# Kernel optimization log

Measured on AMD Instinct MI355X. Metric: run time of the kernel, lower is better.

## Reference

```python
import jax, jax.numpy as jnp
import numpy as np

IMAGE_SIZE = 256
VIEW_ANGLE = 30.0 * np.pi / 180.0  # NMR default viewing angle
SIGMA = 1e-2                        # softness of the differentiable coverage test
EPS = 1e-6


def setup_inputs() -> dict:
    key = jax.random.key(0)
    k1, k2, k3 = jax.random.split(key, 3)
    V, F = 502, 1000
    # normalize_vertices -> points on/near the unit sphere centered at origin
    verts = jax.random.normal(k1, (1, V, 3), dtype=jnp.float32)
    verts = verts / (jnp.linalg.norm(verts, axis=-1, keepdims=True) + EPS)
    faces = jax.random.randint(k2, (1, F, 3), 0, V, dtype=jnp.int32)
    camera_position = jnp.array([6.0, 10.0, -14.0], dtype=jnp.float32)
    # binary silhouette reference, as produced by (image.max(-1) > 0.1)
    image_ref = (jax.random.uniform(k3, (1, IMAGE_SIZE, IMAGE_SIZE)) > 0.5).astype(jnp.float32)
    return {"vertices": verts, "faces": faces, "camera_position": camera_position, "image_ref": image_ref}


def _look_at(vertices, eye):
    # camera_mode='look_at': at=origin, up=+y
    at = jnp.zeros(3, dtype=vertices.dtype)
    up = jnp.array([0.0, 1.0, 0.0], dtype=vertices.dtype)
    z = at - eye
    z = z / (jnp.linalg.norm(z) + EPS)
    x = jnp.cross(up, z)
    x = x / (jnp.linalg.norm(x) + EPS)
    y = jnp.cross(z, x)
    R = jnp.stack([x, y, z], axis=0)           # [3,3], rows are camera axes
    return jnp.einsum('bvj,ij->bvi', vertices - eye, R)  # [1,V,3]


def _render_silhouette(vertices, faces, eye):
    H = W = IMAGE_SIZE
    v = _look_at(vertices, eye)                # [1,V,3] camera space
    w = jnp.tan(jnp.asarray(VIEW_ANGLE, v.dtype))
    zc = v[..., 2]
    proj = jnp.stack([v[..., 0] / (zc * w), v[..., 1] / (zc * w)], axis=-1)  # [1,V,2] NDC xy
    fv = proj[0][faces[0]]                     # [F,3,2] projected triangle vertices
    v0, v1, v2 = fv[:, 0], fv[:, 1], fv[:, 2]

    # pixel centers in NDC, row 0 at top (y=+)
    xs = (2.0 * jnp.arange(W, dtype=v.dtype) + 1.0) / W - 1.0
    ys = 1.0 - (2.0 * jnp.arange(H, dtype=v.dtype) + 1.0) / H
    px = jnp.stack(jnp.meshgrid(xs, ys, indexing='xy'), axis=-1).reshape(-1, 2)  # [P,2]

    def edge_sdist(a, b):
        # signed distance of every pixel to line a->b, computed as px @ n^T - (a.n)
        e = b - a                                           # [F,2]
        n = jnp.stack([-e[:, 1], e[:, 0]], axis=-1)
        n = n / (jnp.linalg.norm(e, axis=-1, keepdims=True) + EPS)
        return px @ n.T - jnp.sum(a * n, axis=-1)[None, :]  # [P,F]

    # orient consistently via signed triangle area
    e01, e02 = v1 - v0, v2 - v0
    area = e01[:, 0] * e02[:, 1] - e01[:, 1] * e02[:, 0]    # [F]
    s = jnp.sign(area)[None, :]

    inv_sigma = 1.0 / SIGMA
    frag = (jax.nn.sigmoid(edge_sdist(v0, v1) * s * inv_sigma)
            * jax.nn.sigmoid(edge_sdist(v1, v2) * s * inv_sigma)
            * jax.nn.sigmoid(edge_sdist(v2, v0) * s * inv_sigma))  # [P,F] soft coverage

    sil = 1.0 - jnp.prod(1.0 - frag, axis=1)                # soft-or over faces, [P]
    return sil.reshape(1, H, W)


def reference(vertices, faces, camera_position, image_ref):
    image = _render_silhouette(vertices, faces, camera_position)  # [1,H,W]
    loss = jnp.sum((image - image_ref) ** 2)
    return loss
```

## Files before the change

### kernel.cpp

```cpp
#include <hip/hip_runtime.h>
#include <math.h>

#define IMG 256
#define NPIX (IMG*IMG)
#define SIGMA_INV 100.0f
#define EPSF 1e-6f
#define LOG2E 1.4426950408889634f
#define TANV 0.5773502691896258f
#define TSKIP 24.0f
#define FMAX 1024
#define NWAVE 8
#define NTILE 1024
#define NCHUNK 4
#define NSBLK (NTILE*NCHUNK)
#define NLBLK 128

__device__ __forceinline__ float fexp2(float x) {
#if __has_builtin(__builtin_amdgcn_exp2f)
  return __builtin_amdgcn_exp2f(x);
#else
  return exp2f(x);
#endif
}
__device__ __forceinline__ float frcp(float x) {
#if __has_builtin(__builtin_amdgcn_rcpf)
  return __builtin_amdgcn_rcpf(x);
#else
  return 1.0f / x;
#endif
}
__device__ __forceinline__ float rlane(float x, int j) {
#if __has_builtin(__builtin_amdgcn_readlane)
  return __int_as_float(__builtin_amdgcn_readlane(__float_as_int(x), j));
#else
  return __shfl(x, j);
#endif
}

__device__ __forceinline__ float cross2(float ax, float ay, float bx, float by) {
#pragma clang fp contract(off)
  return ax * by - ay * bx;
}

__global__ void prep_kernel(const float* __restrict__ verts,
                            const int* __restrict__ faces,
                            const float* __restrict__ cam,
                            float4* __restrict__ fd0, float4* __restrict__ fd1,
                            float4* __restrict__ fd2, int F) {
  int f = blockIdx.x * blockDim.x + threadIdx.x;
  if (f >= F) return;
  float ex = cam[0], ey = cam[1], ez = cam[2];
  float zn = sqrtf(ex * ex + ey * ey + ez * ez) + EPSF;
  float izn = frcp(zn);
  float zx = -ex * izn, zy = -ey * izn, zz = -ez * izn;
  float xn = sqrtf(zz * zz + zx * zx) + EPSF;
  float ixn = frcp(xn);
  float xx = zz * ixn, xz = -zx * ixn;
  float yx = zy * xz;
  float yy = zz * xx - zx * xz;
  float yz = -zy * xx;

  int i0 = faces[3 * f + 0], i1 = faces[3 * f + 1], i2 = faces[3 * f + 2];
  bool deg = (i0 == i1) | (i1 == i2) | (i0 == i2);
  int vi_[3] = {i0, i1, i2};

  float pxs[3], pys[3];
#pragma unroll
  for (int k = 0; k < 3; ++k) {
    int vi = vi_[k];
    float ax = verts[3 * vi + 0] - ex;
    float ay = verts[3 * vi + 1] - ey;
    float az = verts[3 * vi + 2] - ez;
    float vx = ax * xx + az * xz;
    float vy = ax * yx + ay * yy + az * yz;
    float vz = ax * zx + ay * zy + az * zz;
    float izw = frcp(vz * TANV);
    pxs[k] = vx * izw;
    pys[k] = vy * izw;
  }
  float e01x = pxs[1] - pxs[0], e01y = pys[1] - pys[0];
  float e02x = pxs[2] - pxs[0], e02y = pys[2] - pys[0];
  float area = cross2(e01x, e01y, e02x, e02y);
  float s = deg ? 0.0f
                : ((area > 0.0f) ? 1.0f : ((area < 0.0f) ? -1.0f : 0.0f));
  float K = -s * SIGMA_INV * LOG2E;
  float4 o[3];
#pragma unroll
  for (int k = 0; k < 3; ++k) {
    int kn = (k == 2) ? 0 : k + 1;
    float dx = pxs[kn] - pxs[k], dy = pys[kn] - pys[k];
    float il = frcp(sqrtf(dx * dx + dy * dy) + EPSF);
    float nx = -dy * il, ny = dx * il;
    float c = pxs[k] * nx + pys[k] * ny;
    o[k] = make_float4(nx * K, ny * K, -c * K, 0.0f);
  }
  fd0[f] = o[0]; fd1[f] = o[1]; fd2[f] = o[2];
}

__global__ __launch_bounds__(512) void sil_kernel(
    const float4* __restrict__ fd0, const float4* __restrict__ fd1,
    const float4* __restrict__ fd2, float* __restrict__ part,
    int F, int cpf, int fpw) {
  __shared__ float s_part[NWAVE * 64];

  int q = (blockIdx.x * 1021) & (NSBLK - 1);
  int tile = q >> 2, chunk = q & 3;
  int tid = threadIdx.x;
  int lane = tid & 63, w = tid >> 6;
  int bx = tile & 31, by = tile >> 5;
  int ix = (bx << 3) + (lane & 7);
  int iy = (by << 3) + (lane >> 3);
  float px = (2.0f * (float)ix + 1.0f) * (1.0f / IMG) - 1.0f;
  float py = 1.0f - (2.0f * (float)iy + 1.0f) * (1.0f / IMG);
  float cx = ((float)(16 * bx + 8)) * (1.0f / IMG) - 1.0f;
  float cy = 1.0f - ((float)(16 * by + 8)) * (1.0f / IMG);
  const float h = 7.0f / IMG;

  int c0 = chunk * cpf;
  int cF = c0 + cpf; if (cF > F) cF = F;
  int f0 = c0 + w * fpw;
  int f1 = f0 + fpw; if (f1 > cF) f1 = cF;

  float acc = 1.0f;
  for (int base = f0; base < f1; base += 64) {
    int f = base + lane;
    int idx = f < F ? f : F - 1;
    float4 a0 = fd0[idx];
    float4 a1 = fd1[idx];
    float4 a2 = fd2[idx];
    float m0 = fmaf(cx, a0.x, fmaf(cy, a0.y, a0.z)) - (fabsf(a0.x) + fabsf(a0.y)) * h;
    float m1 = fmaf(cx, a1.x, fmaf(cy, a1.y, a1.z)) - (fabsf(a1.x) + fabsf(a1.y)) * h;
    float m2 = fmaf(cx, a2.x, fmaf(cy, a2.y, a2.z)) - (fabsf(a2.x) + fabsf(a2.y)) * h;
    bool rel = (f < f1) && (fmaxf(m0, fmaxf(m1, m2)) < TSKIP);
    unsigned long long mask = __ballot(rel ? 1 : 0);
    while (mask) {
      int j = __builtin_ctzll(mask);
      mask &= mask - 1;
      float b0x = rlane(a0.x, j), b0y = rlane(a0.y, j), b0z = rlane(a0.z, j);
      float b1x = rlane(a1.x, j), b1y = rlane(a1.y, j), b1z = rlane(a1.z, j);
      float b2x = rlane(a2.x, j), b2y = rlane(a2.y, j), b2z = rlane(a2.z, j);
      float t0 = fmaf(px, b0x, fmaf(py, b0y, b0z));
      float t1 = fmaf(px, b1x, fmaf(py, b1y, b1z));
      float t2 = fmaf(px, b2x, fmaf(py, b2y, b2z));
      float D = (1.0f + fexp2(t0)) * (1.0f + fexp2(t1)) * (1.0f + fexp2(t2));
      acc = fmaf(-frcp(D), acc, acc);
    }
  }

  s_part[w * 64 + lane] = acc;
  __syncthreads();

  if (w == 0) {
    float p = 1.0f;
#pragma unroll
    for (int c = 0; c < NWAVE; ++c) p *= s_part[c * 64 + lane];
    part[chunk * NPIX + iy * IMG + ix] = p;
  }
}

__global__ __launch_bounds__(512) void loss_kernel(const float* __restrict__ part,
                                                   const float* __restrict__ ref,
                                                   float* __restrict__ bsum) {
  int p = blockIdx.x * 512 + threadIdx.x;
  float a = part[p] * part[p + NPIX] * part[p + 2 * NPIX] * part[p + 3 * NPIX];
  float d = (1.0f - a) - ref[p];
  float v = d * d;
#pragma unroll
  for (int off = 32; off > 0; off >>= 1) v += __shfl_down(v, off);
  __shared__ float red[8];
  if ((threadIdx.x & 63) == 0) red[threadIdx.x >> 6] = v;
  __syncthreads();
  if (threadIdx.x == 0) {
    float t = 0.0f;
#pragma unroll
    for (int c = 0; c < 8; ++c) t += red[c];
    bsum[blockIdx.x] = t;
  }
}

__global__ __launch_bounds__(128) void reduce_kernel(const float* __restrict__ bsum,
                                                     float* __restrict__ out) {
  int tid = threadIdx.x;
  float v = (tid < NLBLK) ? bsum[tid] : 0.0f;
#pragma unroll
  for (int off = 32; off > 0; off >>= 1) v += __shfl_down(v, off);
  __shared__ float red[2];
  if ((tid & 63) == 0) red[tid >> 6] = v;
  __syncthreads();
  if (tid == 0) out[0] = red[0] + red[1];
}

extern "C" void kernel_launch(void* const* d_in, const int* in_sizes, int n_in,
                              void* d_out, int out_size, void* d_ws, size_t ws_size,
                              hipStream_t stream) {
  const float* verts = (const float*)d_in[0];
  const int* faces = (const int*)d_in[1];
  const float* cam = (const float*)d_in[2];
  const float* imref = (const float*)d_in[3];
  int V = in_sizes[0] / 3;  (void)V;
  int F = in_sizes[1] / 3;
  float* out = (float*)d_out;

  char* ws = (char*)d_ws;
  float4* fd0 = (float4*)(ws + 0 * FMAX * 16);
  float4* fd1 = (float4*)(ws + 1 * FMAX * 16);
  float4* fd2 = (float4*)(ws + 2 * FMAX * 16);
  float* part = (float*)(ws + 65536);
  float* bsum = (float*)(ws + 65536 + NCHUNK * NPIX * 4);

  prep_kernel<<<(F + 255) / 256, 256, 0, stream>>>(verts, faces, cam,
                                                   fd0, fd1, fd2, F);
  int cpf = (F + NCHUNK - 1) / NCHUNK;
  int fpw = (cpf + NWAVE - 1) / NWAVE;
  sil_kernel<<<NSBLK, 512, 0, stream>>>(fd0, fd1, fd2, part, F, cpf, fpw);
  loss_kernel<<<NLBLK, 512, 0, stream>>>(part, imref, bsum);
  reduce_kernel<<<1, 128, 0, stream>>>(bsum, out);
}
```

Measured before the change: 84.80 us.

## Fuse face prep into silhouette kernel and reduce via atomicAdd

Removes the separate face-preprocessing kernel: each silhouette block now recomputes projected edge coefficients for its own 64 faces per wave, 256 faces per group, 4 groups. Blocks shrink to 256 threads with one face batch per wave. The final reduction kernel is replaced by a memset plus an atomicAdd from each loss block. This trades redundant per-block projection math (every tile recomputes all face data) for fewer kernel launches and no intermediate face buffer. It also assumes F is at most 1024 and makes the float summation order nondeterministic.

New measurement: 89.42 us. 1.05x slower.

```diff
diff --git a/kernel.cpp b/kernel.cpp
--- a/kernel.cpp
+++ b/kernel.cpp
@@ -8,11 +8,8 @@
 #define LOG2E 1.4426950408889634f
 #define TANV 0.5773502691896258f
 #define TSKIP 24.0f
-#define FMAX 1024
-#define NWAVE 8
-#define NTILE 1024
-#define NCHUNK 4
-#define NSBLK (NTILE*NCHUNK)
+#define NGROUP 4
+#define NSBLK (1024*NGROUP)
 #define NLBLK 128
 
 __device__ __forceinline__ float fexp2(float x) {
@@ -42,13 +39,27 @@
   return ax * by - ay * bx;
 }
 
-__global__ void prep_kernel(const float* __restrict__ verts,
-                            const int* __restrict__ faces,
-                            const float* __restrict__ cam,
-                            float4* __restrict__ fd0, float4* __restrict__ fd1,
-                            float4* __restrict__ fd2, int F) {
-  int f = blockIdx.x * blockDim.x + threadIdx.x;
-  if (f >= F) return;
+__global__ __launch_bounds__(256) void sil_kernel(
+    const float* __restrict__ verts, const int* __restrict__ faces,
+    const float* __restrict__ cam, float* __restrict__ part, int F) {
+  __shared__ float s_part[NGROUP * 64];
+
+  int q = (blockIdx.x * 1637) & (NSBLK - 1);
+  int tile = q >> 2, group = q & 3;
+  int tid = threadIdx.x;
+  int lane = tid & 63, w = tid >> 6;
+  int bx = tile & 31, by = tile >> 5;
+  int ix = (bx << 3) + (lane & 7);
+  int iy = (by << 3) + (lane >> 3);
+  float px = (2.0f * (float)ix + 1.0f) * (1.0f / IMG) - 1.0f;
+  float py = 1.0f - (2.0f * (float)iy + 1.0f) * (1.0f / IMG);
+  float cx = ((float)(16 * bx + 8)) * (1.0f / IMG) - 1.0f;
+  float cy = 1.0f - ((float)(16 * by + 8)) * (1.0f / IMG);
+  const float h = 7.0f / IMG;
+
+  int f = (group * 4 + w) * 64 + lane;
+  int fc = (f < F) ? f : F - 1;
+
   float ex = cam[0], ey = cam[1], ez = cam[2];
   float zn = sqrtf(ex * ex + ey * ey + ez * ez) + EPSF;
   float izn = frcp(zn);
@@ -60,10 +71,9 @@
   float yy = zz * xx - zx * xz;
   float yz = -zy * xx;
 
-  int i0 = faces[3 * f + 0], i1 = faces[3 * f + 1], i2 = faces[3 * f + 2];
+  int i0 = faces[3 * fc + 0], i1 = faces[3 * fc + 1], i2 = faces[3 * fc + 2];
   bool deg = (i0 == i1) | (i1 == i2) | (i0 == i2);
   int vi_[3] = {i0, i1, i2};
-
   float pxs[3], pys[3];
 #pragma unroll
   for (int k = 0; k < 3; ++k) {
@@ -84,7 +94,7 @@
   float s = deg ? 0.0f
                 : ((area > 0.0f) ? 1.0f : ((area < 0.0f) ? -1.0f : 0.0f));
   float K = -s * SIGMA_INV * LOG2E;
-  float4 o[3];
+  float c0x, c0y, c0z, c1x, c1y, c1z, c2x, c2y, c2z;
 #pragma unroll
   for (int k = 0; k < 3; ++k) {
     int kn = (k == 2) ? 0 : k + 1;
@@ -92,75 +102,45 @@
     float il = frcp(sqrtf(dx * dx + dy * dy) + EPSF);
     float nx = -dy * il, ny = dx * il;
     float c = pxs[k] * nx + pys[k] * ny;
-    o[k] = make_float4(nx * K, ny * K, -c * K, 0.0f);
+    float ox = nx * K, oy = ny * K, oz = -c * K;
+    if (k == 0) { c0x = ox; c0y = oy; c0z = oz; }
+    else if (k == 1) { c1x = ox; c1y = oy; c1z = oz; }
+    else { c2x = ox; c2y = oy; c2z = oz; }
   }
-  fd0[f] = o[0]; fd1[f] = o[1]; fd2[f] = o[2];
-}
 
-__global__ __launch_bounds__(512) void sil_kernel(
-    const float4* __restrict__ fd0, const float4* __restrict__ fd1,
-    const float4* __restrict__ fd2, float* __restrict__ part,
-    int F, int cpf, int fpw) {
-  __shared__ float s_part[NWAVE * 64];
-
-  int q = (blockIdx.x * 1021) & (NSBLK - 1);
-  int tile = q >> 2, chunk = q & 3;
-  int tid = threadIdx.x;
-  int lane = tid & 63, w = tid >> 6;
-  int bx = tile & 31, by = tile >> 5;
-  int ix = (bx << 3) + (lane & 7);
-  int iy = (by << 3) + (lane >> 3);
-  float px = (2.0f * (float)ix + 1.0f) * (1.0f / IMG) - 1.0f;
-  float py = 1.0f - (2.0f * (float)iy + 1.0f) * (1.0f / IMG);
-  float cx = ((float)(16 * bx + 8)) * (1.0f / IMG) - 1.0f;
-  float cy = 1.0f - ((float)(16 * by + 8)) * (1.0f / IMG);
-  const float h = 7.0f / IMG;
-
-  int c0 = chunk * cpf;
-  int cF = c0 + cpf; if (cF > F) cF = F;
-  int f0 = c0 + w * fpw;
-  int f1 = f0 + fpw; if (f1 > cF) f1 = cF;
+  float m0 = fmaf(cx, c0x, fmaf(cy, c0y, c0z)) - (fabsf(c0x) + fabsf(c0y)) * h;
+  float m1 = fmaf(cx, c1x, fmaf(cy, c1y, c1z)) - (fabsf(c1x) + fabsf(c1y)) * h;
+  float m2 = fmaf(cx, c2x, fmaf(cy, c2y, c2z)) - (fabsf(c2x) + fabsf(c2y)) * h;
+  bool rel = (f < F) && (fmaxf(m0, fmaxf(m1, m2)) < TSKIP);
+  unsigned long long mask = __ballot(rel ? 1 : 0);
 
   float acc = 1.0f;
-  for (int base = f0; base < f1; base += 64) {
-    int f = base + lane;
-    int idx = f < F ? f : F - 1;
-    float4 a0 = fd0[idx];
-    float4 a1 = fd1[idx];
-    float4 a2 = fd2[idx];
-    float m0 = fmaf(cx, a0.x, fmaf(cy, a0.y, a0.z)) - (fabsf(a0.x) + fabsf(a0.y)) * h;
-    float m1 = fmaf(cx, a1.x, fmaf(cy, a1.y, a1.z)) - (fabsf(a1.x) + fabsf(a1.y)) * h;
-    float m2 = fmaf(cx, a2.x, fmaf(cy, a2.y, a2.z)) - (fabsf(a2.x) + fabsf(a2.y)) * h;
-    bool rel = (f < f1) && (fmaxf(m0, fmaxf(m1, m2)) < TSKIP);
-    unsigned long long mask = __ballot(rel ? 1 : 0);
-    while (mask) {
-      int j = __builtin_ctzll(mask);
-      mask &= mask - 1;
-      float b0x = rlane(a0.x, j), b0y = rlane(a0.y, j), b0z = rlane(a0.z, j);
-      float b1x = rlane(a1.x, j), b1y = rlane(a1.y, j), b1z = rlane(a1.z, j);
-      float b2x = rlane(a2.x, j), b2y = rlane(a2.y, j), b2z = rlane(a2.z, j);
-      float t0 = fmaf(px, b0x, fmaf(py, b0y, b0z));
-      float t1 = fmaf(px, b1x, fmaf(py, b1y, b1z));
-      float t2 = fmaf(px, b2x, fmaf(py, b2y, b2z));
-      float D = (1.0f + fexp2(t0)) * (1.0f + fexp2(t1)) * (1.0f + fexp2(t2));
-      acc = fmaf(-frcp(D), acc, acc);
-    }
+  while (mask) {
+    int j = __builtin_ctzll(mask);
+    mask &= mask - 1;
+    float b0x = rlane(c0x, j), b0y = rlane(c0y, j), b0z = rlane(c0z, j);
+    float b1x = rlane(c1x, j), b1y = rlane(c1y, j), b1z = rlane(c1z, j);
+    float b2x = rlane(c2x, j), b2y = rlane(c2y, j), b2z = rlane(c2z, j);
+    float t0 = fmaf(px, b0x, fmaf(py, b0y, b0z));
+    float t1 = fmaf(px, b1x, fmaf(py, b1y, b1z));
+    float t2 = fmaf(px, b2x, fmaf(py, b2y, b2z));
+    float D = (1.0f + fexp2(t0)) * (1.0f + fexp2(t1)) * (1.0f + fexp2(t2));
+    acc = fmaf(-frcp(D), acc, acc);
   }
 
   s_part[w * 64 + lane] = acc;
   __syncthreads();
 
   if (w == 0) {
-    float p = 1.0f;
-#pragma unroll
-    for (int c = 0; c < NWAVE; ++c) p *= s_part[c * 64 + lane];
-    part[chunk * NPIX + iy * IMG + ix] = p;
+    float p = s_part[lane] * s_part[64 + lane] *
+              s_part[128 + lane] * s_part[192 + lane];
+    part[group * NPIX + iy * IMG + ix] = p;
   }
 }
 
 __global__ __launch_bounds__(512) void loss_kernel(const float* __restrict__ part,
                                                    const float* __restrict__ ref,
-                                                   float* __restrict__ bsum) {
+                                                   float* __restrict__ out) {
   int p = blockIdx.x * 512 + threadIdx.x;
   float a = part[p] * part[p + NPIX] * part[p + 2 * NPIX] * part[p + 3 * NPIX];
   float d = (1.0f - a) - ref[p];
@@ -174,20 +154,8 @@
     float t = 0.0f;
 #pragma unroll
     for (int c = 0; c < 8; ++c) t += red[c];
-    bsum[blockIdx.x] = t;
+    atomicAdd(out, t);
   }
-}
-
-__global__ __launch_bounds__(128) void reduce_kernel(const float* __restrict__ bsum,
-                                                     float* __restrict__ out) {
-  int tid = threadIdx.x;
-  float v = (tid < NLBLK) ? bsum[tid] : 0.0f;
-#pragma unroll
-  for (int off = 32; off > 0; off >>= 1) v += __shfl_down(v, off);
-  __shared__ float red[2];
-  if ((tid & 63) == 0) red[tid >> 6] = v;
-  __syncthreads();
-  if (tid == 0) out[0] = red[0] + red[1];
 }
 
 extern "C" void kernel_launch(void* const* d_in, const int* in_sizes, int n_in,
@@ -200,19 +168,9 @@
   int V = in_sizes[0] / 3;  (void)V;
   int F = in_sizes[1] / 3;
   float* out = (float*)d_out;
+  float* part = (float*)d_ws;
 
-  char* ws = (char*)d_ws;
-  float4* fd0 = (float4*)(ws + 0 * FMAX * 16);
-  float4* fd1 = (float4*)(ws + 1 * FMAX * 16);
-  float4* fd2 = (float4*)(ws + 2 * FMAX * 16);
-  float* part = (float*)(ws + 65536);
-  float* bsum = (float*)(ws + 65536 + NCHUNK * NPIX * 4);
-
-  prep_kernel<<<(F + 255) / 256, 256, 0, stream>>>(verts, faces, cam,
-                                                   fd0, fd1, fd2, F);
-  int cpf = (F + NCHUNK - 1) / NCHUNK;
-  int fpw = (cpf + NWAVE - 1) / NWAVE;
-  sil_kernel<<<NSBLK, 512, 0, stream>>>(fd0, fd1, fd2, part, F, cpf, fpw);
-  loss_kernel<<<NLBLK, 512, 0, stream>>>(part, imref, bsum);
-  reduce_kernel<<<1, 128, 0, stream>>>(bsum, out);
+  hipMemsetAsync(out, 0, sizeof(float), stream);
+  sil_kernel<<<NSBLK, 256, 0, stream>>>(verts, faces, cam, part, F);
+  loss_kernel<<<NLBLK, 512, 0, stream>>>(part, imref, out);
 }
```

## Shrink silhouette blocks to four waves and fold final reduction into atomics

Applied to the files above, without the earlier changes.

The silhouette kernel now uses 256-thread blocks where each wave handles exactly one 64-face slice of its chunk, which removes the per-wave face loop and lets every block load its face data once. The final reduce kernel is removed: the prep kernel zeroes the output and the loss kernel accumulates its block sums with atomicAdd. This cuts one kernel launch and the loop overhead, and halves the threads per block. The atomic float accumulation makes the summation order nondeterministic, and the code assumes a chunk holds at most 256 faces (F at most 1024).

Result: no change. 83.84 us (-1.1%).

```diff
diff --git a/kernel.cpp b/kernel.cpp
--- a/kernel.cpp
+++ b/kernel.cpp
@@ -9,9 +9,8 @@
 #define TANV 0.5773502691896258f
 #define TSKIP 24.0f
 #define FMAX 1024
-#define NWAVE 8
+#define NCHUNK 4
 #define NTILE 1024
-#define NCHUNK 4
 #define NSBLK (NTILE*NCHUNK)
 #define NLBLK 128
 
@@ -46,8 +45,10 @@
                             const int* __restrict__ faces,
                             const float* __restrict__ cam,
                             float4* __restrict__ fd0, float4* __restrict__ fd1,
-                            float4* __restrict__ fd2, int F) {
+                            float4* __restrict__ fd2, float* __restrict__ out,
+                            int F) {
   int f = blockIdx.x * blockDim.x + threadIdx.x;
+  if (f == 0) out[0] = 0.0f;
   if (f >= F) return;
   float ex = cam[0], ey = cam[1], ez = cam[2];
   float zn = sqrtf(ex * ex + ey * ey + ez * ez) + EPSF;
@@ -97,13 +98,13 @@
   fd0[f] = o[0]; fd1[f] = o[1]; fd2[f] = o[2];
 }
 
-__global__ __launch_bounds__(512) void sil_kernel(
+__global__ __launch_bounds__(256) void sil_kernel(
     const float4* __restrict__ fd0, const float4* __restrict__ fd1,
     const float4* __restrict__ fd2, float* __restrict__ part,
-    int F, int cpf, int fpw) {
-  __shared__ float s_part[NWAVE * 64];
+    int F, int cpf) {
+  __shared__ float s_part[NCHUNK * 64];
 
-  int q = (blockIdx.x * 1021) & (NSBLK - 1);
+  int q = (blockIdx.x * 1637) & (NSBLK - 1);
   int tile = q >> 2, chunk = q & 3;
   int tid = threadIdx.x;
   int lane = tid & 63, w = tid >> 6;
@@ -116,51 +117,45 @@
   float cy = 1.0f - ((float)(16 * by + 8)) * (1.0f / IMG);
   const float h = 7.0f / IMG;
 
-  int c0 = chunk * cpf;
-  int cF = c0 + cpf; if (cF > F) cF = F;
-  int f0 = c0 + w * fpw;
-  int f1 = f0 + fpw; if (f1 > cF) f1 = cF;
+  int r = w * 64 + lane;
+  int f = chunk * cpf + r;
+  int idx = (f < F) ? f : F - 1;
+  float4 a0 = fd0[idx];
+  float4 a1 = fd1[idx];
+  float4 a2 = fd2[idx];
+  float m0 = fmaf(cx, a0.x, fmaf(cy, a0.y, a0.z)) - (fabsf(a0.x) + fabsf(a0.y)) * h;
+  float m1 = fmaf(cx, a1.x, fmaf(cy, a1.y, a1.z)) - (fabsf(a1.x) + fabsf(a1.y)) * h;
+  float m2 = fmaf(cx, a2.x, fmaf(cy, a2.y, a2.z)) - (fabsf(a2.x) + fabsf(a2.y)) * h;
+  bool rel = (r < cpf) && (f < F) && (fmaxf(m0, fmaxf(m1, m2)) < TSKIP);
+  unsigned long long mask = __ballot(rel ? 1 : 0);
 
   float acc = 1.0f;
-  for (int base = f0; base < f1; base += 64) {
-    int f = base + lane;
-    int idx = f < F ? f : F - 1;
-    float4 a0 = fd0[idx];
-    float4 a1 = fd1[idx];
-    float4 a2 = fd2[idx];
-    float m0 = fmaf(cx, a0.x, fmaf(cy, a0.y, a0.z)) - (fabsf(a0.x) + fabsf(a0.y)) * h;
-    float m1 = fmaf(cx, a1.x, fmaf(cy, a1.y, a1.z)) - (fabsf(a1.x) + fabsf(a1.y)) * h;
-    float m2 = fmaf(cx, a2.x, fmaf(cy, a2.y, a2.z)) - (fabsf(a2.x) + fabsf(a2.y)) * h;
-    bool rel = (f < f1) && (fmaxf(m0, fmaxf(m1, m2)) < TSKIP);
-    unsigned long long mask = __ballot(rel ? 1 : 0);
-    while (mask) {
-      int j = __builtin_ctzll(mask);
-      mask &= mask - 1;
-      float b0x = rlane(a0.x, j), b0y = rlane(a0.y, j), b0z = rlane(a0.z, j);
-      float b1x = rlane(a1.x, j), b1y = rlane(a1.y, j), b1z = rlane(a1.z, j);
-      float b2x = rlane(a2.x, j), b2y = rlane(a2.y, j), b2z = rlane(a2.z, j);
-      float t0 = fmaf(px, b0x, fmaf(py, b0y, b0z));
-      float t1 = fmaf(px, b1x, fmaf(py, b1y, b1z));
-      float t2 = fmaf(px, b2x, fmaf(py, b2y, b2z));
-      float D = (1.0f + fexp2(t0)) * (1.0f + fexp2(t1)) * (1.0f + fexp2(t2));
-      acc = fmaf(-frcp(D), acc, acc);
-    }
+  while (mask) {
+    int j = __builtin_ctzll(mask);
+    mask &= mask - 1;
+    float b0x = rlane(a0.x, j), b0y = rlane(a0.y, j), b0z = rlane(a0.z, j);
+    float b1x = rlane(a1.x, j), b1y = rlane(a1.y, j), b1z = rlane(a1.z, j);
+    float b2x = rlane(a2.x, j), b2y = rlane(a2.y, j), b2z = rlane(a2.z, j);
+    float t0 = fmaf(px, b0x, fmaf(py, b0y, b0z));
+    float t1 = fmaf(px, b1x, fmaf(py, b1y, b1z));
+    float t2 = fmaf(px, b2x, fmaf(py, b2y, b2z));
+    float D = (1.0f + fexp2(t0)) * (1.0f + fexp2(t1)) * (1.0f + fexp2(t2));
+    acc = fmaf(-frcp(D), acc, acc);
   }
 
   s_part[w * 64 + lane] = acc;
   __syncthreads();
 
   if (w == 0) {
-    float p = 1.0f;
-#pragma unroll
-    for (int c = 0; c < NWAVE; ++c) p *= s_part[c * 64 + lane];
+    float p = s_part[lane] * s_part[64 + lane] *
+              s_part[128 + lane] * s_part[192 + lane];
     part[chunk * NPIX + iy * IMG + ix] = p;
   }
 }
 
 __global__ __launch_bounds__(512) void loss_kernel(const float* __restrict__ part,
                                                    const float* __restrict__ ref,
-                                                   float* __restrict__ bsum) {
+                                                   float* __restrict__ out) {
   int p = blockIdx.x * 512 + threadIdx.x;
   float a = part[p] * part[p + NPIX] * part[p + 2 * NPIX] * part[p + 3 * NPIX];
   float d = (1.0f - a) - ref[p];
@@ -174,20 +169,8 @@
     float t = 0.0f;
 #pragma unroll
     for (int c = 0; c < 8; ++c) t += red[c];
-    bsum[blockIdx.x] = t;
+    atomicAdd(out, t);
   }
-}
-
-__global__ __launch_bounds__(128) void reduce_kernel(const float* __restrict__ bsum,
-                                                     float* __restrict__ out) {
-  int tid = threadIdx.x;
-  float v = (tid < NLBLK) ? bsum[tid] : 0.0f;
-#pragma unroll
-  for (int off = 32; off > 0; off >>= 1) v += __shfl_down(v, off);
-  __shared__ float red[2];
-  if ((tid & 63) == 0) red[tid >> 6] = v;
-  __syncthreads();
-  if (tid == 0) out[0] = red[0] + red[1];
 }
 
 extern "C" void kernel_launch(void* const* d_in, const int* in_sizes, int n_in,
@@ -206,13 +189,10 @@
   float4* fd1 = (float4*)(ws + 1 * FMAX * 16);
   float4* fd2 = (float4*)(ws + 2 * FMAX * 16);
   float* part = (float*)(ws + 65536);
-  float* bsum = (float*)(ws + 65536 + NCHUNK * NPIX * 4);
 
   prep_kernel<<<(F + 255) / 256, 256, 0, stream>>>(verts, faces, cam,
-                                                   fd0, fd1, fd2, F);
+                                                   fd0, fd1, fd2, out, F);
   int cpf = (F + NCHUNK - 1) / NCHUNK;
-  int fpw = (cpf + NWAVE - 1) / NWAVE;
-  sil_kernel<<<NSBLK, 512, 0, stream>>>(fd0, fd1, fd2, part, F, cpf, fpw);
-  loss_kernel<<<NLBLK, 512, 0, stream>>>(part, imref, bsum);
-  reduce_kernel<<<1, 128, 0, stream>>>(bsum, out);
+  sil_kernel<<<NSBLK, 256, 0, stream>>>(fd0, fd1, fd2, part, F, cpf);
+  loss_kernel<<<NLBLK, 512, 0, stream>>>(part, imref, out);
 }
```
